# Kernel tuning notes

Measured on AMD Instinct MI355X. Metric: run time of the kernel, lower is better.

Reference implementation:

```python
import jax, jax.numpy as jnp
import numpy as np
from math import sqrt

L, H, D, HD, F, V, P = 8, 16, 1024, 64, 4096, 32000, 2048
B, S = 2, 2048
EPS = 1e-5


def _ln(x, g, b):
    m = jnp.mean(x, axis=-1, keepdims=True)
    v = jnp.mean((x - m) ** 2, axis=-1, keepdims=True)
    return (x - m) * jax.lax.rsqrt(v + EPS) * g + b


def setup_inputs() -> dict:
    key = jax.random.key(0)
    ks = jax.random.split(key, 12)
    w = 0.02
    return {
        'input_ids': jax.random.randint(ks[0], (B, S), 0, V),
        'tok_emb': jax.random.normal(ks[1], (V, D), jnp.float32) * w,
        'pos_emb': jax.random.normal(ks[2], (P, D), jnp.float32) * w,
        'emb_g': jnp.ones((D,), jnp.float32),
        'emb_b': jnp.zeros((D,), jnp.float32),
        'ln1_g': jnp.ones((L, D), jnp.float32),
        'ln1_b': jnp.zeros((L, D), jnp.float32),
        'ln2_g': jnp.ones((L, D), jnp.float32),
        'ln2_b': jnp.zeros((L, D), jnp.float32),
        'Wq': jax.random.normal(ks[3], (L, H, D, HD), jnp.float32) * w,
        'bq': jnp.zeros((L, H, HD), jnp.float32),
        'Wk': jax.random.normal(ks[4], (L, H, D, HD), jnp.float32) * w,
        'bk': jnp.zeros((L, H, HD), jnp.float32),
        'Wv': jax.random.normal(ks[5], (L, H, D, HD), jnp.float32) * w,
        'bv': jnp.zeros((L, H, HD), jnp.float32),
        'Wo': jax.random.normal(ks[6], (L, D, D), jnp.float32) * w,
        'bo': jnp.zeros((L, D), jnp.float32),
        'W1': jax.random.normal(ks[7], (L, D, F), jnp.float32) * w,
        'b1': jnp.zeros((L, F), jnp.float32),
        'W2': jax.random.normal(ks[8], (L, F, D), jnp.float32) * w,
        'b2': jnp.zeros((L, D), jnp.float32),
    }


def _encoder(input_ids, tok_emb, pos_emb, emb_g, emb_b, ln1_g, ln1_b, ln2_g,
             ln2_b, Wq, bq, Wk, bk, Wv, bv, Wo, bo, W1, b1, W2, b2):
    seq = input_ids.shape[-1]
    x = tok_emb[input_ids] + pos_emb[:seq][None, :, :]  # [B,S,D]
    x = _ln(x, emb_g, emb_b)  # dropout = identity (eval)

    scale = 1.0 / sqrt(HD)

    def layer(x, p):
        (g1, b1_, g2, b2_, wq, bq_, wk, bk_, wv, bv_, wo, bo_, w1, bb1, w2, bb2) = p
        h = _ln(x, g1, b1_)
        q = jnp.einsum('bsd,hdk->bhsk', h, wq) + bq_[:, None, :]
        k = jnp.einsum('bsd,hdk->bhsk', h, wk) + bk_[:, None, :]
        v = jnp.einsum('bsd,hdk->bhsk', h, wv) + bv_[:, None, :]
        scores = jnp.einsum('bhsk,bhtk->bhst', q, k) * scale
        w = jax.nn.softmax(scores, axis=-1)
        av = jnp.einsum('bhst,bhtk->bhsk', w, v)  # [B,H,S,hd]
        av = jnp.transpose(av, (0, 2, 1, 3)).reshape(x.shape[0], x.shape[1], D)
        x = x + jnp.einsum('bsd,de->bse', av, wo) + bo_
        h2 = _ln(x, g2, b2_)
        f = jax.nn.gelu(jnp.einsum('bsd,df->bsf', h2, w1) + bb1, approximate=False)
        x = x + jnp.einsum('bsf,fd->bsd', f, w2) + bb2
        return x, None

    xs = (ln1_g, ln1_b, ln2_g, ln2_b, Wq, bq, Wk, bk, Wv, bv, Wo, bo, W1, b1, W2, b2)
    x, _ = jax.lax.scan(layer, x, xs)
    return x


def reference(input_ids, tok_emb, pos_emb, emb_g, emb_b, ln1_g, ln1_b, ln2_g,
              ln2_b, Wq, bq, Wk, bk, Wv, bv, Wo, bo, W1, b1, W2, b2):
    return _encoder(input_ids, tok_emb, pos_emb, emb_g, emb_b, ln1_g, ln1_b,
                    ln2_g, ln2_b, Wq, bq, Wk, bk, Wv, bv, Wo, bo, W1, b1, W2, b2)
```

## Files before the change

kernel.cpp:

```cpp
#include <hip/hip_runtime.h>
#include <hip/hip_bf16.h>

#define L_ 8
#define H_ 16
#define D_ 1024
#define HD_ 64
#define F_ 4096
#define B_ 2
#define S_ 2048
#define NTOK (B_*S_)

typedef unsigned short u16;
typedef __bf16 bf16x8 __attribute__((ext_vector_type(8)));
typedef float f32x4 __attribute__((ext_vector_type(4)));

__device__ __forceinline__ u16 f2b(float f){ union{float f; unsigned u;} c; c.f = f; unsigned u = c.u; return (u16)((u + 0x7fffu + ((u>>16)&1u)) >> 16); }
__device__ __forceinline__ u16 f2b_fast(float f){ union{float f; unsigned u;} c; c.f = f; return (u16)((c.u + 0x8000u) >> 16); }
__device__ __forceinline__ float b2f(u16 x){ union{unsigned u; float f;} c; c.u = ((unsigned)x)<<16; return c.f; }

__device__ __forceinline__ void gload16(const u16* g, u16* l){
  __builtin_amdgcn_global_load_lds(
      (const __attribute__((address_space(1))) void*)g,
      (__attribute__((address_space(3))) void*)l,
      16 , 0 , 0 );
}

#define WAITV_BAR(n) do { \
  asm volatile("s_waitcnt vmcnt(%0)" :: "i"(n) : "memory"); \
  __builtin_amdgcn_sched_barrier(0); \
  __builtin_amdgcn_s_barrier(); \
} while(0)

__device__ __forceinline__ void blk_reduce2(float& a, float& b, float* sm){
  for (int off=32; off>0; off>>=1){ a += __shfl_down(a,off); b += __shfl_down(b,off); }
  int w = threadIdx.x>>6, ln = threadIdx.x&63;
  if (ln==0){ sm[w]=a; sm[4+w]=b; }
  __syncthreads();
  a = sm[0]+sm[1]+sm[2]+sm[3];
  b = sm[4]+sm[5]+sm[6]+sm[7];
}

__global__ __launch_bounds__(256) void embed_ln(const int* __restrict__ ids,
    const float* __restrict__ tok, const float* __restrict__ pos,
    const float* __restrict__ g, const float* __restrict__ bb,
    float* __restrict__ x)
{
  __shared__ float sm[8];
  int row = blockIdx.x;
  int s   = row % S_;
  int id  = ids[row];
  int d0  = threadIdx.x*4;
  float4 t4 = *(const float4*)(tok + (size_t)id*D_ + d0);
  float4 p4 = *(const float4*)(pos + (size_t)s *D_ + d0);
  float4 v; v.x=t4.x+p4.x; v.y=t4.y+p4.y; v.z=t4.z+p4.z; v.w=t4.w+p4.w;
  float sum = (v.x+v.y)+(v.z+v.w);
  float sq  = v.x*v.x+v.y*v.y+v.z*v.z+v.w*v.w;
  blk_reduce2(sum, sq, sm);
  float mean = sum * (1.0f/D_);
  float var  = sq  * (1.0f/D_) - mean*mean;
  float inv  = rsqrtf(var + 1e-5f);
  float4 g4 = *(const float4*)(g + d0);
  float4 b4 = *(const float4*)(bb + d0);
  float4 o; o.x=(v.x-mean)*inv*g4.x+b4.x; o.y=(v.y-mean)*inv*g4.y+b4.y;
            o.z=(v.z-mean)*inv*g4.z+b4.z; o.w=(v.w-mean)*inv*g4.w+b4.w;
  *(float4*)(x + (size_t)row*D_ + d0) = o;
}

__global__ __launch_bounds__(256) void ln_f32_bf16(const float* __restrict__ x,
    const float* __restrict__ g, const float* __restrict__ bb, u16* __restrict__ out)
{
  __shared__ float sm[8];
  int row = blockIdx.x;
  int d0  = threadIdx.x*4;
  float4 v = *(const float4*)(x + (size_t)row*D_ + d0);
  float sum = (v.x+v.y)+(v.z+v.w);
  float sq  = v.x*v.x+v.y*v.y+v.z*v.z+v.w*v.w;
  blk_reduce2(sum, sq, sm);
  float mean = sum * (1.0f/D_);
  float var  = sq  * (1.0f/D_) - mean*mean;
  float inv  = rsqrtf(var + 1e-5f);
  float4 g4 = *(const float4*)(g + d0);
  float4 b4 = *(const float4*)(bb + d0);
  uint2 w;
  w.x = (unsigned)f2b((v.x-mean)*inv*g4.x+b4.x) | ((unsigned)f2b((v.y-mean)*inv*g4.y+b4.y)<<16);
  w.y = (unsigned)f2b((v.z-mean)*inv*g4.z+b4.z) | ((unsigned)f2b((v.w-mean)*inv*g4.w+b4.w)<<16);
  *(uint2*)(out + (size_t)row*D_ + d0) = w;
}

__global__ __launch_bounds__(256) void transpose_w(const float* __restrict__ src,
    u16* __restrict__ dst, int R, int C)
{
  __shared__ u16 tile[32][33];
  int c0 = blockIdx.x*32, r0 = blockIdx.y*32;
  int tx = threadIdx.x, ty = threadIdx.y;
  #pragma unroll
  for (int i=0;i<4;i++){
    int r = ty + i*8;
    tile[r][tx] = f2b(src[(size_t)(r0+r)*C + c0 + tx]);
  }
  __syncthreads();
  #pragma unroll
  for (int i=0;i<4;i++){
    int c = ty + i*8;
    dst[(size_t)(c0+c)*R + r0 + tx] = tile[tx][c];
  }
}

__global__ __launch_bounds__(256) void qkv_repack(const float* __restrict__ Wq,
    const float* __restrict__ Wk, const float* __restrict__ Wv,
    u16* __restrict__ dst, int layer)
{
  __shared__ u16 tile[32][33];
  int z = blockIdx.z; int which = z >> 4, h = z & 15;
  const float* W = (which==0) ? Wq : (which==1) ? Wk : Wv;
  const float* src = W + ((size_t)(layer*H_ + h))*D_*HD_;
  int d0 = blockIdx.x*32, c0 = blockIdx.y*32;
  int tx = threadIdx.x, ty = threadIdx.y;
  #pragma unroll
  for (int i=0;i<4;i++){
    int r = ty + i*8;
    tile[r][tx] = f2b(src[(size_t)(d0+r)*HD_ + c0 + tx]);
  }
  __syncthreads();
  #pragma unroll
  for (int i=0;i<4;i++){
    int hd = c0 + ty + i*8;
    dst[(size_t)(which*1024 + h*64 + hd)*D_ + d0 + tx] = tile[tx][ty + i*8];
  }
}

__global__ __launch_bounds__(256) void v_transpose(const u16* __restrict__ qkv, u16* __restrict__ vT)
{
  __shared__ u16 tile[64*64];
  const int tt = blockIdx.x;
  const int bh = blockIdx.y;
  const int b = bh>>4, h = bh&15;
  const int t = threadIdx.x;
  const u16* src = qkv + (size_t)(b*S_ + tt*64)*3072 + 2048 + h*64;
  #pragma unroll
  for (int i=0;i<2;i++){
    int idx = t + i*256;
    int tl = idx>>3, hc = idx&7;
    uint4 v = *(const uint4*)(src + (size_t)tl*3072 + hc*8);
    *(uint4*)(&tile[tl*64 + ((hc ^ (tl&7))<<3)]) = v;
  }
  __syncthreads();
  u16* dst = vT + ((size_t)bh*64)*S_ + tt*64;
  #pragma unroll
  for (int i=0;i<2;i++){
    int idx = t + i*256;
    int hd = idx>>3, tc = idx&7;
    u16 tmp[8];
    #pragma unroll
    for (int j=0;j<8;j++){
      int tk = tc*8 + j;
      tmp[j] = tile[tk*64 + (hd ^ ((tk&7)<<3))];
    }
    *(uint4*)(dst + (size_t)hd*S_ + tc*8) = *(uint4*)tmp;
  }
}

__device__ __forceinline__ void epi_store(float v0,float v1,float v2,float v3,
    float* xres, u16* obf, size_t idx, int epi)
{
  if (epi==1){
    float4 t = *(float4*)(xres + idx);
    t.x += v0; t.y += v1; t.z += v2; t.w += v3;
    *(float4*)(xres + idx) = t;
  } else {
    if (epi==2){
      #define GELU_T(v) { float t2=(v)*(v); float u=(v)*fmaf(t2,0.044715f,1.0f); \
                          float e=exp2f(u*-2.3022082f); (v)=(v)*__builtin_amdgcn_rcpf(1.0f+e); }
      GELU_T(v0); GELU_T(v1); GELU_T(v2); GELU_T(v3);
      #undef GELU_T
    }
    uint2 w;
    w.x = (unsigned)f2b_fast(v0) | ((unsigned)f2b_fast(v1) << 16);
    w.y = (unsigned)f2b_fast(v2) | ((unsigned)f2b_fast(v3) << 16);
    *(uint2*)(obf + idx) = w;
  }
}

__global__ __launch_bounds__(256) void gemm_bf16(
    const u16* __restrict__ A, const u16* __restrict__ Bt,
    const float* __restrict__ bias0, const float* __restrict__ bias1, const float* __restrict__ bias2,
    float* __restrict__ xres, u16* __restrict__ obf,
    int M, int N, int K, int epi)
{
  __shared__ u16 As[128*64];
  __shared__ u16 Bs[128*64];
  const int tid = threadIdx.x;
  const int nbx = gridDim.x;
  const int nwg = nbx * gridDim.y;
  int bid = blockIdx.x + nbx*blockIdx.y;
  int nid = (bid & 7)*(nwg >> 3) + (bid >> 3);
  const int bm = (nid % nbx) * 128;
  const int bn = (nid / nbx) * 128;
  const int wv = tid>>6, ln = tid&63;
  const int wr = wv>>1, wc = wv&1;
  const int l15 = ln&15, lhi = ln>>4;
  const int l8 = ln>>3;
  const int c8s = (ln&7) ^ l8;
  f32x4 acc[4][4];
  const f32x4 zero4 = {0.f,0.f,0.f,0.f};
  #pragma unroll
  for (int i=0;i<4;i++)
    #pragma unroll
    for (int j=0;j<4;j++) acc[i][j] = zero4;

  for (int k0 = 0; k0 < K; k0 += 64) {
    #pragma unroll
    for (int i=0;i<4;i++){
      int row = wv*8 + i*32 + l8;
      gload16(A  + (size_t)(bm+row)*K + k0 + c8s*8, &As[(wv*8 + i*32)*64]);
      gload16(Bt + (size_t)(bn+row)*K + k0 + c8s*8, &Bs[(wv*8 + i*32)*64]);
    }
    __syncthreads();
    #pragma unroll
    for (int ks=0; ks<2; ks++){
      bf16x8 af[4], bfr[4];
      #pragma unroll
      for (int i=0;i<4;i++){
        int ra = wr*64 + i*16 + l15;
        af[i]  = *(const bf16x8*)(&As[ra*64 + (((ks*4+lhi) ^ (ra&7))<<3)]);
        int rb = wc*64 + i*16 + l15;
        bfr[i] = *(const bf16x8*)(&Bs[rb*64 + (((ks*4+lhi) ^ (rb&7))<<3)]);
      }
      #pragma unroll
      for (int i=0;i<4;i++)
        #pragma unroll
        for (int j=0;j<4;j++)
          acc[i][j] = __builtin_amdgcn_mfma_f32_16x16x32_bf16(bfr[j], af[i], acc[i][j], 0,0,0);
    }
    __syncthreads();
  }

  #pragma unroll
  for (int j=0;j<4;j++){
    int col0 = bn + wc*64 + j*16 + lhi*4;
    float4 bv4;
    if (bias1){
      const float* bp = (col0 < 1024) ? (bias0 + col0)
                      : (col0 < 2048) ? (bias1 + col0 - 1024)
                                      : (bias2 + col0 - 2048);
      bv4 = *(const float4*)bp;
    } else {
      bv4 = *(const float4*)(bias0 + col0);
    }
    #pragma unroll
    for (int i=0;i<4;i++){
      int row = bm + wr*64 + i*16 + l15;
      epi_store(acc[i][j][0]+bv4.x, acc[i][j][1]+bv4.y, acc[i][j][2]+bv4.z, acc[i][j][3]+bv4.w,
                xres, obf, (size_t)row*N + col0, epi);
    }
  }
}

__global__ __launch_bounds__(512,2) void gemm256(
    const u16* __restrict__ A, const u16* __restrict__ Bt,
    const float* __restrict__ bias0, const float* __restrict__ bias1, const float* __restrict__ bias2,
    float* __restrict__ xres, u16* __restrict__ obf,
    int M, int N, int K, int epi)
{
  __shared__ u16 As[2][256*64];
  __shared__ u16 Bs[2][256*64];
  const int tid = threadIdx.x;
  const int nbx = gridDim.x;
  const int nwg = nbx * gridDim.y;
  int bid = blockIdx.x + nbx*blockIdx.y;
  int nid = (bid & 7)*(nwg >> 3) + (bid >> 3);
  const int bm = (nid % nbx) * 256;
  const int bn = (nid / nbx) * 256;
  const int wv = tid>>6, ln = tid&63;
  const int wm = wv>>2, wn = wv&3;
  const int l15 = ln&15, lhi = ln>>4;
  const int l8 = ln>>3;
  const int c8s = (ln&7) ^ l8;

  f32x4 acc[2][2][4][2];
  const f32x4 zero4 = {0.f,0.f,0.f,0.f};
  #pragma unroll
  for (int a=0;a<2;a++)
    #pragma unroll
    for (int b=0;b<2;b++)
      #pragma unroll
      for (int i=0;i<4;i++)
        #pragma unroll
        for (int j=0;j<2;j++) acc[a][b][i][j] = zero4;

  const u16* aB0 = A  + (size_t)(bm + wv*16 + l8)*K + c8s*8;
  const u16* bB0 = Bt + (size_t)(bn + wv*16 + l8)*K + c8s*8;

  #define ISSUE(c, kt) do {                                                  \
    const u16* aB = aB0 + (size_t)(kt)*64;                                   \
    const u16* bB = bB0 + (size_t)(kt)*64;                                   \
    gload16(aB,                 &As[c][(wv*16      )*64]);                   \
    gload16(aB + (size_t)8*K,   &As[c][(wv*16 +   8)*64]);                   \
    gload16(bB,                 &Bs[c][(wv*16      )*64]);                   \
    gload16(bB + (size_t)8*K,   &Bs[c][(wv*16 +   8)*64]);                   \
    gload16(bB + (size_t)128*K, &Bs[c][(128 + wv*16    )*64]);               \
    gload16(bB + (size_t)136*K, &Bs[c][(128 + wv*16 + 8)*64]);               \
    gload16(aB + (size_t)128*K, &As[c][(128 + wv*16    )*64]);               \
    gload16(aB + (size_t)136*K, &As[c][(128 + wv*16 + 8)*64]);               \
  } while(0)

  #define READ_B(c) do {                                                     \
    _Pragma("unroll")                                                        \
    for (int qc=0;qc<2;qc++)                                                 \
      _Pragma("unroll")                                                      \
      for (int j=0;j<2;j++){                                                 \
        int rb = qc*128 + wn*32 + j*16 + l15;                                \
        _Pragma("unroll")                                                    \
        for (int ks=0;ks<2;ks++)                                             \
          bfr[qc][j][ks] = *(const bf16x8*)(&Bs[c][rb*64 + (((ks*4+lhi) ^ (rb&7))<<3)]); \
      }                                                                      \
  } while(0)

  #define READ_A(c, qr) do {                                                 \
    _Pragma("unroll")                                                        \
    for (int i=0;i<4;i++){                                                   \
      int ra = (qr)*128 + wm*64 + i*16 + l15;                                \
      _Pragma("unroll")                                                      \
      for (int ks=0;ks<2;ks++)                                               \
        af[i][ks] = *(const bf16x8*)(&As[c][ra*64 + (((ks*4+lhi) ^ (ra&7))<<3)]); \
    }                                                                        \
  } while(0)

  #define MFMA_Q(qr) do {                                                    \
    __builtin_amdgcn_s_setprio(1);                                           \
    _Pragma("unroll")                                                        \
    for (int ks=0;ks<2;ks++)                                                 \
      _Pragma("unroll")                                                      \
      for (int i=0;i<4;i++)                                                  \
        _Pragma("unroll")                                                    \
        for (int qc=0;qc<2;qc++)                                             \
          _Pragma("unroll")                                                  \
          for (int j=0;j<2;j++)                                              \
            acc[qr][qc][i][j] = __builtin_amdgcn_mfma_f32_16x16x32_bf16(     \
                bfr[qc][j][ks], af[i][ks], acc[qr][qc][i][j], 0,0,0);        \
    __builtin_amdgcn_s_setprio(0);                                           \
  } while(0)

  const int nt = K >> 6;
  ISSUE(0, 0);
  WAITV_BAR(2);
  for (int t=0; t<nt-1; ++t){
    int c = t&1;
    ISSUE(c^1, t+1);
    bf16x8 bfr[2][2][2], af[4][2];
    READ_B(c);
    READ_A(c, 0);
    MFMA_Q(0);
    WAITV_BAR(8);
    READ_A(c, 1);
    MFMA_Q(1);
    WAITV_BAR(2);
  }
  {
    int c = (nt-1)&1;
    bf16x8 bfr[2][2][2], af[4][2];
    READ_B(c);
    READ_A(c, 0);
    MFMA_Q(0);
    WAITV_BAR(0);
    READ_A(c, 1);
    MFMA_Q(1);
  }
  #undef ISSUE
  #undef READ_B
  #undef READ_A
  #undef MFMA_Q

  #pragma unroll
  for (int qc=0; qc<2; qc++)
    #pragma unroll
    for (int j=0;j<2;j++){
      int col0 = bn + qc*128 + wn*32 + j*16 + lhi*4;
      float4 bv4;
      if (bias1){
        const float* bp = (col0 < 1024) ? (bias0 + col0)
                        : (col0 < 2048) ? (bias1 + col0 - 1024)
                                        : (bias2 + col0 - 2048);
        bv4 = *(const float4*)bp;
      } else {
        bv4 = *(const float4*)(bias0 + col0);
      }
      #pragma unroll
      for (int qr=0; qr<2; qr++)
        #pragma unroll
        for (int i=0;i<4;i++){
          int row = bm + qr*128 + wm*64 + i*16 + l15;
          epi_store(acc[qr][qc][i][j][0]+bv4.x, acc[qr][qc][i][j][1]+bv4.y,
                    acc[qr][qc][i][j][2]+bv4.z, acc[qr][qc][i][j][3]+bv4.w,
                    xres, obf, (size_t)row*N + col0, epi);
        }
    }
}

__global__ __launch_bounds__(256) void attn_fwd(const u16* __restrict__ qkv,
    const u16* __restrict__ vT, u16* __restrict__ att)
{
  __shared__ u16 Ks[2][64*64];
  __shared__ u16 Vs[2][64*64];
  const int tid = threadIdx.x, wv = tid>>6, ln = tid&63, l15 = ln&15, lhi = ln>>4;
  const int l8 = ln>>3;
  const int cs = (ln&7) ^ l8;
  int bid = blockIdx.x + 16*(blockIdx.y + 16*blockIdx.z);
  int nid = (bid & 7)*64 + (bid >> 3);
  const int qt = nid & 15, h = (nid >> 4) & 15, b = nid >> 8;
  const u16* qg = qkv + (size_t)b*S_*3072 + h*64;
  const u16* kg = qg + 1024;
  const u16* vtg = vT + ((size_t)(b*16 + h)*64)*S_;

  bf16x8 qfA[2], qfB[2];
  {
    const u16* qrA = qg + (size_t)(qt*128 + wv*32 + l15)*3072;
    const u16* qrB = qrA + (size_t)16*3072;
    u16 ta[16], tb[16];
    *(uint4*)(ta)   = *(const uint4*)(qrA + lhi*8);
    *(uint4*)(ta+8) = *(const uint4*)(qrA + 32 + lhi*8);
    *(uint4*)(tb)   = *(const uint4*)(qrB + lhi*8);
    *(uint4*)(tb+8) = *(const uint4*)(qrB + 32 + lhi*8);
    #pragma unroll
    for (int i=0;i<16;i++){ ta[i] = f2b_fast(b2f(ta[i]) * 0.18033688f);
                            tb[i] = f2b_fast(b2f(tb[i]) * 0.18033688f); }
    qfA[0] = *(const bf16x8*)(ta); qfA[1] = *(const bf16x8*)(ta+8);
    qfB[0] = *(const bf16x8*)(tb); qfB[1] = *(const bf16x8*)(tb+8);
  }
  const f32x4 zero4 = {0.f,0.f,0.f,0.f};
  f32x4 oaccA[4], oaccB[4];
  #pragma unroll
  for (int j=0;j<4;j++){ oaccA[j] = zero4; oaccB[j] = zero4; }
  float lsumA = 0.f, lsumB = 0.f;

  #define STAGE_KV(bufi, kti) do {                                            \
    _Pragma("unroll")                                                         \
    for (int i_=0;i_<2;i_++){                                                 \
      int r0_ = wv*8 + i_*32;                                                 \
      int row_ = r0_ + l8;                                                    \
      gload16(kg  + (size_t)((kti)*64+row_)*3072 + cs*8, &Ks[bufi][r0_*64]);  \
      gload16(vtg + (size_t)row_*S_ + (kti)*64 + cs*8,   &Vs[bufi][r0_*64]);  \
    }                                                                         \
  } while(0)

  #define EXCHANGE(pk, pf) do {                                               \
    _Pragma("unroll")                                                         \
    for (int ks=0; ks<2; ks++){                                               \
      unsigned pw[4];                                                         \
      _Pragma("unroll")                                                       \
      for (int w=0; w<4; w++){                                                \
        int src = l15 + (lhi&1)*32 + (w>>1)*16;                               \
        unsigned a  = __shfl(pk[ks*4 + (w&1)],     src);                      \
        unsigned bb2 = __shfl(pk[ks*4 + 2 + (w&1)], src);                     \
        pw[w] = (lhi & 2) ? bb2 : a;                                          \
      }                                                                       \
      union { unsigned u[4]; bf16x8 v; } pu;                                  \
      pu.u[0]=pw[0]; pu.u[1]=pw[1]; pu.u[2]=pw[2]; pu.u[3]=pw[3];             \
      pf[ks] = pu.v;                                                          \
    }                                                                         \
  } while(0)

  STAGE_KV(0, 0);
  __syncthreads();
  int buf = 0;

  for (int kt=0; kt<S_/64; kt++){
    if (kt+1 < S_/64) STAGE_KV(buf^1, kt+1);

    f32x4 sA[4], sB[4];
    __builtin_amdgcn_s_setprio(1);
    #pragma unroll
    for (int j=0;j<4;j++){
      sA[j] = zero4; sB[j] = zero4;
      #pragma unroll
      for (int ks=0; ks<2; ks++){
        int kr = j*16 + l15;
        bf16x8 kf = *(const bf16x8*)(&Ks[buf][kr*64 + (((ks*4+lhi) ^ (kr&7))<<3)]);
        sA[j] = __builtin_amdgcn_mfma_f32_16x16x32_bf16(kf, qfA[ks], sA[j], 0,0,0);
        sB[j] = __builtin_amdgcn_mfma_f32_16x16x32_bf16(kf, qfB[ks], sB[j], 0,0,0);
      }
    }
    __builtin_amdgcn_s_setprio(0);

    unsigned pkA[8], pkB[8];
    float partA = 0.f, partB = 0.f;
    #pragma unroll
    for (int j=0;j<4;j++){
      float a0 = exp2f(sA[j][0]), a1 = exp2f(sA[j][1]), a2 = exp2f(sA[j][2]), a3 = exp2f(sA[j][3]);
      float b0 = exp2f(sB[j][0]), b1 = exp2f(sB[j][1]), b2 = exp2f(sB[j][2]), b3 = exp2f(sB[j][3]);
      partA += (a0+a1)+(a2+a3);
      partB += (b0+b1)+(b2+b3);
      asm("v_cvt_pk_bf16_f32 %0, %1, %2" : "=v"(pkA[j*2])   : "v"(a0), "v"(a1));
      asm("v_cvt_pk_bf16_f32 %0, %1, %2" : "=v"(pkA[j*2+1]) : "v"(a2), "v"(a3));
      asm("v_cvt_pk_bf16_f32 %0, %1, %2" : "=v"(pkB[j*2])   : "v"(b0), "v"(b1));
      asm("v_cvt_pk_bf16_f32 %0, %1, %2" : "=v"(pkB[j*2+1]) : "v"(b2), "v"(b3));
    }
    lsumA += partA; lsumB += partB;

    bf16x8 pfA[2], pfB[2];
    EXCHANGE(pkA, pfA);
    EXCHANGE(pkB, pfB);

    __builtin_amdgcn_s_setprio(1);
    #pragma unroll
    for (int dj=0; dj<4; dj++){
      #pragma unroll
      for (int ks=0; ks<2; ks++){
        int vr = dj*16 + l15;
        bf16x8 vf = *(const bf16x8*)(&Vs[buf][vr*64 + (((ks*4+lhi) ^ (vr&7))<<3)]);
        oaccA[dj] = __builtin_amdgcn_mfma_f32_16x16x32_bf16(pfA[ks], vf, oaccA[dj], 0,0,0);
        oaccB[dj] = __builtin_amdgcn_mfma_f32_16x16x32_bf16(pfB[ks], vf, oaccB[dj], 0,0,0);
      }
    }
    __builtin_amdgcn_s_setprio(0);
    __syncthreads();
    buf ^= 1;
  }
  #undef STAGE_KV
  #undef EXCHANGE

  float totA = lsumA + __shfl_xor(lsumA, 16); totA += __shfl_xor(totA, 32);
  float totB = lsumB + __shfl_xor(lsumB, 16); totB += __shfl_xor(totB, 32);
  float invA[4], invB[4];
  #pragma unroll
  for (int r=0;r<4;r++){
    invA[r] = __builtin_amdgcn_rcpf(__shfl(totA, lhi*4+r));
    invB[r] = __builtin_amdgcn_rcpf(__shfl(totB, lhi*4+r));
  }

  #pragma unroll
  for (int dj=0; dj<4; dj++){
    #pragma unroll
    for (int r=0;r<4;r++){
      int q = lhi*4 + r;
      int tokA = qt*128 + wv*32 + q;
      int tokB = tokA + 16;
      att[(size_t)(b*S_ + tokA)*D_ + h*HD_ + dj*16 + l15] = f2b_fast(oaccA[dj][r] * invA[r]);
      att[(size_t)(b*S_ + tokB)*D_ + h*HD_ + dj*16 + l15] = f2b_fast(oaccB[dj][r] * invB[r]);
    }
  }
}

extern "C" void kernel_launch(void* const* d_in, const int* in_sizes, int n_in,
                              void* d_out, int out_size, void* d_ws, size_t ws_size,
                              hipStream_t stream)
{
  const int*   ids   = (const int*)d_in[0];
  const float* tok   = (const float*)d_in[1];
  const float* pos   = (const float*)d_in[2];
  const float* emb_g = (const float*)d_in[3];
  const float* emb_b = (const float*)d_in[4];
  const float* ln1g  = (const float*)d_in[5];
  const float* ln1b  = (const float*)d_in[6];
  const float* ln2g  = (const float*)d_in[7];
  const float* ln2b  = (const float*)d_in[8];
  const float* Wq = (const float*)d_in[9];
  const float* bq = (const float*)d_in[10];
  const float* Wk = (const float*)d_in[11];
  const float* bk = (const float*)d_in[12];
  const float* Wv = (const float*)d_in[13];
  const float* bv = (const float*)d_in[14];
  const float* Wo = (const float*)d_in[15];
  const float* bo = (const float*)d_in[16];
  const float* W1 = (const float*)d_in[17];
  const float* b1 = (const float*)d_in[18];
  const float* W2 = (const float*)d_in[19];
  const float* b2 = (const float*)d_in[20];

  float* x = (float*)d_out;
  char* ws = (char*)d_ws;
  u16* h     = (u16*)(ws);
  u16* qkvb  = (u16*)(ws + 8388608);
  u16* att   = (u16*)(ws + 33554432);
  u16* fbuf  = (u16*)(ws + 41943040);
  u16* vT    = fbuf;
  u16* wqkvt = (u16*)(ws + 75497472);
  u16* wot   = (u16*)(ws + 81788928);
  u16* w1t   = (u16*)(ws + 83886080);
  u16* w2t   = (u16*)(ws + 92274688);

  embed_ln<<<NTOK, 256, 0, stream>>>(ids, tok, pos, emb_g, emb_b, x);

  for (int l=0; l<L_; l++){
    ln_f32_bf16<<<NTOK, 256, 0, stream>>>(x, ln1g + l*D_, ln1b + l*D_, h);
    qkv_repack<<<dim3(32,2,48), dim3(32,8), 0, stream>>>(Wq, Wk, Wv, wqkvt, l);
    gemm256<<<dim3(16,12), 512, 0, stream>>>(h, wqkvt,
        bq + l*1024, bk + l*1024, bv + l*1024,
        nullptr, qkvb, NTOK, 3072, 1024, 0);
    v_transpose<<<dim3(32,32), 256, 0, stream>>>(qkvb, vT);
    attn_fwd<<<dim3(S_/128, H_, B_), 256, 0, stream>>>(qkvb, vT, att);
    transpose_w<<<dim3(32,32), dim3(32,8), 0, stream>>>(Wo + (size_t)l*D_*D_, wot, D_, D_);
    gemm_bf16<<<dim3(32,8), 256, 0, stream>>>(att, wot,
        bo + l*D_, nullptr, nullptr,
        x, nullptr, NTOK, 1024, 1024, 1);
    ln_f32_bf16<<<NTOK, 256, 0, stream>>>(x, ln2g + l*D_, ln2b + l*D_, h);
    transpose_w<<<dim3(128,32), dim3(32,8), 0, stream>>>(W1 + (size_t)l*D_*F_, w1t, D_, F_);
    gemm256<<<dim3(16,16), 512, 0, stream>>>(h, w1t,
        b1 + l*F_, nullptr, nullptr,
        nullptr, fbuf, NTOK, 4096, 1024, 2);
    transpose_w<<<dim3(32,128), dim3(32,8), 0, stream>>>(W2 + (size_t)l*F_*D_, w2t, F_, D_);
    gemm_bf16<<<dim3(32,8), 256, 0, stream>>>(fbuf, w2t,
        b2 + l*D_, nullptr, nullptr,
        x, nullptr, NTOK, 1024, 4096, 1);
  }
}
```

Before: 2.422 ms.

## Split-K the residual-add GEMMs with atomic accumulation into the residual

Replaces the 128x128 residual GEMM (output projection and FFN down projection) with a split-K variant that launches 2 or 4 K-slices along grid z. Each slice atomically adds its partial sums into the fp32 residual, and only slice 0 adds the bias. The aim is to fill the GPU better than the 256 workgroups of the original launch. In exchange it issues many more scalar float atomics, and the summation order becomes nondeterministic.

```diff
diff --git a/kernel.cpp b/kernel.cpp
--- a/kernel.cpp
+++ b/kernel.cpp
@@ -181,11 +181,10 @@
   }
 }
 
-__global__ __launch_bounds__(256) void gemm_bf16(
+__global__ __launch_bounds__(256) void gemm_splitk(
     const u16* __restrict__ A, const u16* __restrict__ Bt,
-    const float* __restrict__ bias0, const float* __restrict__ bias1, const float* __restrict__ bias2,
-    float* __restrict__ xres, u16* __restrict__ obf,
-    int M, int N, int K, int epi)
+    const float* __restrict__ bias0, float* __restrict__ xres,
+    int M, int N, int K, int klen)
 {
   __shared__ u16 As[128*64];
   __shared__ u16 Bs[128*64];
@@ -196,6 +195,8 @@
   int nid = (bid & 7)*(nwg >> 3) + (bid >> 3);
   const int bm = (nid % nbx) * 128;
   const int bn = (nid / nbx) * 128;
+  const int split = blockIdx.z;
+  const int kbeg = split * klen;
   const int wv = tid>>6, ln = tid&63;
   const int wr = wv>>1, wc = wv&1;
   const int l15 = ln&15, lhi = ln>>4;
@@ -208,7 +209,7 @@
     #pragma unroll
     for (int j=0;j<4;j++) acc[i][j] = zero4;
 
-  for (int k0 = 0; k0 < K; k0 += 64) {
+  for (int k0 = kbeg; k0 < kbeg + klen; k0 += 64) {
     #pragma unroll
     for (int i=0;i<4;i++){
       int row = wv*8 + i*32 + l8;
@@ -238,20 +239,16 @@
   #pragma unroll
   for (int j=0;j<4;j++){
     int col0 = bn + wc*64 + j*16 + lhi*4;
-    float4 bv4;
-    if (bias1){
-      const float* bp = (col0 < 1024) ? (bias0 + col0)
-                      : (col0 < 2048) ? (bias1 + col0 - 1024)
-                                      : (bias2 + col0 - 2048);
-      bv4 = *(const float4*)bp;
-    } else {
-      bv4 = *(const float4*)(bias0 + col0);
-    }
+    float4 bv4 = {0.f,0.f,0.f,0.f};
+    if (split == 0) bv4 = *(const float4*)(bias0 + col0);
     #pragma unroll
     for (int i=0;i<4;i++){
       int row = bm + wr*64 + i*16 + l15;
-      epi_store(acc[i][j][0]+bv4.x, acc[i][j][1]+bv4.y, acc[i][j][2]+bv4.z, acc[i][j][3]+bv4.w,
-                xres, obf, (size_t)row*N + col0, epi);
+      size_t idx = (size_t)row*N + col0;
+      atomicAdd(xres + idx + 0, acc[i][j][0] + bv4.x);
+      atomicAdd(xres + idx + 1, acc[i][j][1] + bv4.y);
+      atomicAdd(xres + idx + 2, acc[i][j][2] + bv4.z);
+      atomicAdd(xres + idx + 3, acc[i][j][3] + bv4.w);
     }
   }
 }
@@ -590,17 +587,15 @@
     v_transpose<<<dim3(32,32), 256, 0, stream>>>(qkvb, vT);
     attn_fwd<<<dim3(S_/128, H_, B_), 256, 0, stream>>>(qkvb, vT, att);
     transpose_w<<<dim3(32,32), dim3(32,8), 0, stream>>>(Wo + (size_t)l*D_*D_, wot, D_, D_);
-    gemm_bf16<<<dim3(32,8), 256, 0, stream>>>(att, wot,
-        bo + l*D_, nullptr, nullptr,
-        x, nullptr, NTOK, 1024, 1024, 1);
+    gemm_splitk<<<dim3(32,8,2), 256, 0, stream>>>(att, wot,
+        bo + l*D_, x, NTOK, 1024, 1024, 512);
     ln_f32_bf16<<<NTOK, 256, 0, stream>>>(x, ln2g + l*D_, ln2b + l*D_, h);
     transpose_w<<<dim3(128,32), dim3(32,8), 0, stream>>>(W1 + (size_t)l*D_*F_, w1t, D_, F_);
     gemm256<<<dim3(16,16), 512, 0, stream>>>(h, w1t,
         b1 + l*F_, nullptr, nullptr,
         nullptr, fbuf, NTOK, 4096, 1024, 2);
     transpose_w<<<dim3(32,128), dim3(32,8), 0, stream>>>(W2 + (size_t)l*F_*D_, w2t, F_, D_);
-    gemm_bf16<<<dim3(32,8), 256, 0, stream>>>(fbuf, w2t,
-        b2 + l*D_, nullptr, nullptr,
-        x, nullptr, NTOK, 1024, 4096, 1);
-  }
-}
+    gemm_splitk<<<dim3(32,8,4), 256, 0, stream>>>(fbuf, w2t,
+        b2 + l*D_, x, NTOK, 1024, 4096, 1024);
+  }
+}
```

Result: slower. 4.318 ms (+78.3%).
